# Kernel optimization log

Measured on AMD Instinct MI355X. Metric: run time of the kernel, lower is better.

Reference implementation:

```python
import jax, jax.numpy as jnp
import numpy as np

B, N, D = 4, 2048, 1024
HEADS, DIM_HEAD = 16, 64
INNER = HEADS * DIM_HEAD  # 1024
SCALE = DIM_HEAD ** -0.5


def setup_inputs() -> dict:
    key = jax.random.key(0)
    ks = jax.random.split(key, 8)
    w = 0.02
    return {
        "x":  jax.random.normal(ks[0], (B, N, D), dtype=jnp.float32),
        "Wq": jax.random.normal(ks[1], (D, INNER), dtype=jnp.float32) * w,
        "bq": jax.random.normal(ks[2], (INNER,), dtype=jnp.float32) * w,
        "Wv": jax.random.normal(ks[3], (D, INNER), dtype=jnp.float32) * w,
        "bv": jax.random.normal(ks[4], (INNER,), dtype=jnp.float32) * w,
        "Wo": jax.random.normal(ks[5], (INNER, D), dtype=jnp.float32) * w,
        "bo": jax.random.normal(ks[6], (D,), dtype=jnp.float32) * w,
    }


def reference(x, Wq, bq, Wv, bv, Wo, bo):
    b, n, _ = x.shape
    q = x @ Wq + bq                      # [b, n, inner]
    v = x @ Wv + bv                      # [b, n, inner]
    # split heads -> [b, h, n, d]
    q = q.reshape(b, n, HEADS, DIM_HEAD).transpose(0, 2, 1, 3).astype(jnp.float32)
    v = v.reshape(b, n, HEADS, DIM_HEAD).transpose(0, 2, 1, 3)
    # k = q (self L2 attention)
    AB = jnp.einsum('bhid,bhjd->bhij', q, q)          # [b, h, n, n]
    AA = jnp.sum(q * q, axis=-1, keepdims=True)       # [b, h, n, 1]
    BB = jnp.swapaxes(AA, -1, -2)                     # [b, h, 1, n]
    sim = -(AA - 2.0 * AB + BB) * SCALE               # negative scaled L2 distance
    attn = jax.nn.softmax(sim, axis=-1)
    out = jnp.einsum('bhij,bhjd->bhid', attn, v)      # [b, h, n, d]
    out = out.transpose(0, 2, 1, 3).reshape(b, n, INNER)
    return out @ Wo + bo
```

## Files before the change

### kernel.cpp

```cpp
#include <hip/hip_runtime.h>
#include <hip/hip_bf16.h>

#define SEQ 2048
#define SCALE 0.125f
#define LOG2E 1.4426950408889634f
#define ALPHA 0.6005612049f

typedef __bf16 bf16;
typedef __bf16 bf16x4 __attribute__((ext_vector_type(4)));
typedef __bf16 bf16x8 __attribute__((ext_vector_type(8)));
typedef _Float16 f16;
typedef _Float16 f16x2 __attribute__((ext_vector_type(2)));
typedef _Float16 f16x4 __attribute__((ext_vector_type(4)));
typedef _Float16 f16x8 __attribute__((ext_vector_type(8)));
typedef float f32x4 __attribute__((ext_vector_type(4)));
typedef unsigned int u32;
typedef unsigned int u32x2 __attribute__((ext_vector_type(2)));
typedef unsigned int u32x4 __attribute__((ext_vector_type(4)));

__device__ __forceinline__ f16x2 pk_f16(float a, float b) {
    return __builtin_bit_cast(f16x2, __builtin_amdgcn_cvt_pkrtz(a, b));
}

__device__ __forceinline__ u32 pk_u32(float a, float b) {
    return __builtin_bit_cast(u32, __builtin_amdgcn_cvt_pkrtz(a, b));
}

__device__ __forceinline__ f32x4 mfma_f16_32(f16x8 a, f16x8 b, f32x4 c) {
    return __builtin_amdgcn_mfma_f32_16x16x32_f16(a, b, c, 0, 0, 0);
}

__device__ __forceinline__ void gl_lds16(const void* g, void* l) {
    __builtin_amdgcn_global_load_lds((const __attribute__((address_space(1))) u32*)g,
                                     (__attribute__((address_space(3))) u32*)l, 16, 0, 0);
}


__global__ __launch_bounds__(256) void k_cast_x(const float4* __restrict__ x,
                                                bf16x4* __restrict__ xb) {
    int t = blockIdx.x * 256 + threadIdx.x;
    float4 f = x[t];
    bf16x4 o;
    o[0] = (bf16)f.x; o[1] = (bf16)f.y; o[2] = (bf16)f.z; o[3] = (bf16)f.w;
    xb[t] = o;
}

__global__ __launch_bounds__(256) void k_transpose_cast(const float* __restrict__ src,
                                                        bf16* __restrict__ dst) {
    __shared__ float tile[32][33];
    int bx = blockIdx.x * 32;
    int by = blockIdx.y * 32;
    int tx = threadIdx.x;
    int ty = threadIdx.y;
#pragma unroll
    for (int j = 0; j < 32; j += 8)
        tile[ty + j][tx] = src[(size_t)(by + ty + j) * 1024 + bx + tx];
    __syncthreads();
#pragma unroll
    for (int j = 0; j < 32; j += 8)
        dst[(size_t)(bx + ty + j) * 1024 + by + tx] = (bf16)tile[tx][ty + j];
}


__global__ __launch_bounds__(256) void k_gemm_qv(const bf16* __restrict__ Xb,
                                                 const bf16* __restrict__ Wqvt,
                                                 const float* __restrict__ bq,
                                                 const float* __restrict__ bv,
                                                 bf16* __restrict__ Q,
                                                 f16* __restrict__ Vt,
                                                 float* __restrict__ QN) {
    constexpr int K = 1024;
    __shared__ bf16 As[128 * 32];
    __shared__ bf16 Bs[128 * 32];
    int t = threadIdx.x, w = t >> 6, l = t & 63;
    int blockN = blockIdx.x * 128, blockM = blockIdx.y * 128;
    int wm = w & 1, wn = w >> 1;
    int lr = l & 15, quad = l >> 4, q8 = quad * 8;
    int skcol = (l & 3) * 8;
    bool isQ = blockN < 1024;

    f32x4 acc[4][4] = {};
    const bf16* Ab = Xb + (size_t)blockM * K;
    const bf16* Bb = Wqvt + (size_t)blockN * K;

    for (int k0 = 0; k0 < K; k0 += 32) {
#pragma unroll
        for (int c2 = 0; c2 < 2; ++c2) {
            int c = 2 * w + c2;
            int row = c * 16 + (l >> 2);
            gl_lds16(Ab + (size_t)row * K + k0 + skcol, As + c * 512);
            gl_lds16(Bb + (size_t)row * K + k0 + skcol, Bs + c * 512);
        }
        __syncthreads();
        const bf16* Aw = As + wm * 64 * 32;
        const bf16* Bw = Bs + wn * 64 * 32;
        bf16x8 af[4], bfr[4];
#pragma unroll
        for (int mi = 0; mi < 4; ++mi) af[mi] = *(const bf16x8*)(Aw + (mi * 16 + lr) * 32 + q8);
#pragma unroll
        for (int ni = 0; ni < 4; ++ni) bfr[ni] = *(const bf16x8*)(Bw + (ni * 16 + lr) * 32 + q8);
        if (isQ) {
#pragma unroll
            for (int mi = 0; mi < 4; ++mi)
#pragma unroll
                for (int ni = 0; ni < 4; ++ni)
                    acc[mi][ni] = __builtin_amdgcn_mfma_f32_16x16x32_bf16(af[mi], bfr[ni], acc[mi][ni], 0, 0, 0);
        } else {
#pragma unroll
            for (int mi = 0; mi < 4; ++mi)
#pragma unroll
                for (int ni = 0; ni < 4; ++ni)
                    acc[mi][ni] = __builtin_amdgcn_mfma_f32_16x16x32_bf16(bfr[ni], af[mi], acc[mi][ni], 0, 0, 0);
        }
        __syncthreads();
    }

    int colbase = blockN + wn * 64;
    if (isQ) {
        int h = colbase >> 6;
        float bias[4];
#pragma unroll
        for (int ni = 0; ni < 4; ++ni) bias[ni] = bq[colbase + ni * 16 + lr];
#pragma unroll
        for (int mi = 0; mi < 4; ++mi) {
#pragma unroll
            for (int r = 0; r < 4; ++r) {
                int m = blockM + wm * 64 + mi * 16 + quad * 4 + r;
                int b = m >> 11, s = m & 2047;
                int bh = (b << 4) + h;
                float qsq = 0.f;
#pragma unroll
                for (int ni = 0; ni < 4; ++ni) {
                    float v = (acc[mi][ni][r] + bias[ni]) * ALPHA;
                    bf16 vb = (bf16)v;
                    Q[((size_t)bh * SEQ + s) * 64 + ni * 16 + lr] = vb;
                    float vr = (float)vb;
                    qsq += vr * vr;
                }
                qsq += __shfl_xor(qsq, 1);
                qsq += __shfl_xor(qsq, 2);
                qsq += __shfl_xor(qsq, 4);
                qsq += __shfl_xor(qsq, 8);
                if (lr == 0) QN[(size_t)bh * SEQ + s] = -0.5f * qsq;
            }
        }
    } else {
        int h = (colbase - 1024) >> 6;
        int b = blockM >> 11;
        int bh = (b << 4) + h;
        int s_base = (blockM & 2047) + wm * 64;
        const float* bvh = bv + (colbase - 1024);
#pragma unroll
        for (int ni = 0; ni < 4; ++ni) {
#pragma unroll
            for (int r = 0; r < 4; ++r) {
                int dh = ni * 16 + quad * 4 + r;
                float bias = bvh[dh];
#pragma unroll
                for (int mi = 0; mi < 4; ++mi) {
                    int s = s_base + mi * 16 + lr;
                    Vt[((size_t)bh * 64 + dh) * SEQ + s] = (f16)(acc[mi][ni][r] + bias);
                }
            }
        }
    }
}


__global__ __launch_bounds__(128, 4) void k_attn(const bf16* __restrict__ Q,
                                                 const f16* __restrict__ Vt,
                                                 const float* __restrict__ QN,
                                                 bf16* __restrict__ AO) {
    __shared__ bf16 Ks[64 * 64];
    __shared__ f16 Vs[64 * 64];

    int t = threadIdx.x, w = t >> 6, l = t & 63;
    int bh = blockIdx.y;
    int i0 = blockIdx.x * 64;
    const bf16* Qh = Q + (size_t)bh * SEQ * 64;
    const f16* Vh = Vt + (size_t)bh * 64 * SEQ;
    const float* QNh = QN + (size_t)bh * SEQ;
    int lr = l & 15, quad = l >> 4, q8 = quad * 8, lr7 = lr & 7;

    bf16x8 af[2][2];
#pragma unroll
    for (int mi = 0; mi < 2; ++mi)
#pragma unroll
        for (int kc = 0; kc < 2; ++kc)
            af[mi][kc] = *(const bf16x8*)(Qh + (size_t)(i0 + w * 32 + mi * 16 + lr) * 64 + kc * 32 + q8);

    f32x4 oacc[2][4] = {};
    f32x4 dacc[2] = {};
    const f16x8 ones8 = {(f16)1.f, (f16)1.f, (f16)1.f, (f16)1.f,
                         (f16)1.f, (f16)1.f, (f16)1.f, (f16)1.f};

    int kb[2];
#pragma unroll
    for (int kc = 0; kc < 2; ++kc) kb[kc] = lr * 64 + (((kc * 4 + quad) ^ lr7) * 8);
    int voff[4];
#pragma unroll
    for (int di = 0; di < 4; ++di) voff[di] = (di * 16 + lr) * 64;
    int npo[2];
#pragma unroll
    for (int np = 0; np < 2; ++np) npo[np] = ((np * 4 + quad) ^ lr7) * 8;

    int sr = t >> 3, sc = t & 7;
    int srr[4], sl[4];
#pragma unroll
    for (int i = 0; i < 4; ++i) {
        srr[i] = sr + 16 * i;
        sl[i] = srr[i] * 64 + ((sc ^ (srr[i] & 7)) * 8);
    }

    u32x4 rk[4], rv[4];
#pragma unroll
    for (int i = 0; i < 4; ++i) {
        rk[i] = *(const u32x4*)(Qh + (size_t)srr[i] * 64 + sc * 8);
        rv[i] = *(const u32x4*)(Vh + (size_t)srr[i] * SEQ + sc * 8);
    }

    for (int j0 = 0; j0 < SEQ; j0 += 64) {
        __syncthreads();
#pragma unroll
        for (int i = 0; i < 4; ++i) {
            *(u32x4*)(Ks + sl[i]) = rk[i];
            *(u32x4*)(Vs + sl[i]) = rv[i];
        }
        int jn = j0 + 64;
        if (jn < SEQ) {
#pragma unroll
            for (int i = 0; i < 4; ++i) {
                rk[i] = *(const u32x4*)(Qh + (size_t)(jn + srr[i]) * 64 + sc * 8);
                rv[i] = *(const u32x4*)(Vh + (size_t)srr[i] * SEQ + jn + sc * 8);
            }
        }
        __syncthreads();

#pragma unroll
        for (int np = 0; np < 2; ++np) {
            u32 hA[2][2], hB[2][2];
#pragma unroll
            for (int ni1 = 0; ni1 < 2; ++ni1) {
                int ni = np * 2 + ni1;
                bf16x8 bk0 = *(const bf16x8*)(Ks + ni * 1024 + kb[0]);
                bf16x8 bk1 = *(const bf16x8*)(Ks + ni * 1024 + kb[1]);
                f32x4 bbt = *(const f32x4*)(QNh + j0 + ni * 16 + quad * 4);
                f32x4 sT0 = bbt, sT1 = bbt;
                __builtin_amdgcn_s_setprio(1);
                sT0 = __builtin_amdgcn_mfma_f32_16x16x32_bf16(bk0, af[0][0], sT0, 0, 0, 0);
                sT0 = __builtin_amdgcn_mfma_f32_16x16x32_bf16(bk1, af[0][1], sT0, 0, 0, 0);
                sT1 = __builtin_amdgcn_mfma_f32_16x16x32_bf16(bk0, af[1][0], sT1, 0, 0, 0);
                sT1 = __builtin_amdgcn_mfma_f32_16x16x32_bf16(bk1, af[1][1], sT1, 0, 0, 0);
                __builtin_amdgcn_s_setprio(0);

                float p00 = __builtin_amdgcn_exp2f(sT0[0]);
                float p01 = __builtin_amdgcn_exp2f(sT0[1]);
                float p02 = __builtin_amdgcn_exp2f(sT0[2]);
                float p03 = __builtin_amdgcn_exp2f(sT0[3]);
                float p10 = __builtin_amdgcn_exp2f(sT1[0]);
                float p11 = __builtin_amdgcn_exp2f(sT1[1]);
                float p12 = __builtin_amdgcn_exp2f(sT1[2]);
                float p13 = __builtin_amdgcn_exp2f(sT1[3]);

                hA[ni1][0] = pk_u32(p00, p01);
                hA[ni1][1] = pk_u32(p02, p03);
                hB[ni1][0] = pk_u32(p10, p11);
                hB[ni1][1] = pk_u32(p12, p13);
            }
            f16x8 F8[2];
            {
                u32 a0 = hA[0][0], b0 = hA[1][0], a1 = hA[0][1], b1 = hA[1][1];
                asm("v_permlane32_swap_b32 %0, %1" : "+v"(a0), "+v"(b0));
                asm("v_permlane16_swap_b32 %0, %1" : "+v"(a0), "+v"(b0));
                asm("v_permlane32_swap_b32 %0, %1" : "+v"(a1), "+v"(b1));
                asm("v_permlane16_swap_b32 %0, %1" : "+v"(a1), "+v"(b1));
                u32x4 fu = {a0, a1, b0, b1};
                F8[0] = __builtin_bit_cast(f16x8, fu);
            }
            {
                u32 a0 = hB[0][0], b0 = hB[1][0], a1 = hB[0][1], b1 = hB[1][1];
                asm("v_permlane32_swap_b32 %0, %1" : "+v"(a0), "+v"(b0));
                asm("v_permlane16_swap_b32 %0, %1" : "+v"(a0), "+v"(b0));
                asm("v_permlane32_swap_b32 %0, %1" : "+v"(a1), "+v"(b1));
                asm("v_permlane16_swap_b32 %0, %1" : "+v"(a1), "+v"(b1));
                u32x4 fu = {a0, a1, b0, b1};
                F8[1] = __builtin_bit_cast(f16x8, fu);
            }

            __builtin_amdgcn_s_setprio(1);
            dacc[0] = mfma_f16_32(F8[0], ones8, dacc[0]);
            dacc[1] = mfma_f16_32(F8[1], ones8, dacc[1]);

#pragma unroll
            for (int di = 0; di < 4; ++di) {
                f16x8 vf8 = *(const f16x8*)(Vs + voff[di] + npo[np]);
                oacc[0][di] = mfma_f16_32(F8[0], vf8, oacc[0][di]);
                oacc[1][di] = mfma_f16_32(F8[1], vf8, oacc[1][di]);
            }
            __builtin_amdgcn_s_setprio(0);
        }
    }

    int b = bh >> 4, h = bh & 15;
#pragma unroll
    for (int mi = 0; mi < 2; ++mi) {
#pragma unroll
        for (int r = 0; r < 4; ++r) {
            float inv = 1.f / dacc[mi][r];
            int s = i0 + w * 32 + mi * 16 + quad * 4 + r;
#pragma unroll
            for (int di = 0; di < 4; ++di) {
                AO[((size_t)(b * SEQ + s)) * 1024 + h * 64 + di * 16 + lr] = (bf16)(oacc[mi][di][r] * inv);
            }
        }
    }
}


__global__ __launch_bounds__(256) void k_gemm_out(const bf16* __restrict__ AO,
                                                  const bf16* __restrict__ Wot,
                                                  const float* __restrict__ bo,
                                                  float* __restrict__ out) {
    constexpr int K = 1024;
    __shared__ bf16 As[128 * 32];
    __shared__ bf16 Bs[128 * 32];
    int t = threadIdx.x, w = t >> 6, l = t & 63;
    int blockN = blockIdx.x * 128, blockM = blockIdx.y * 128;
    int wm = w & 1, wn = w >> 1;
    int lr = l & 15, quad = l >> 4, q8 = quad * 8;
    int skcol = (l & 3) * 8;

    f32x4 acc[4][4] = {};
    const bf16* Ab = AO + (size_t)blockM * K;
    const bf16* Bb = Wot + (size_t)blockN * K;

    for (int k0 = 0; k0 < K; k0 += 32) {
#pragma unroll
        for (int c2 = 0; c2 < 2; ++c2) {
            int c = 2 * w + c2;
            int row = c * 16 + (l >> 2);
            gl_lds16(Ab + (size_t)row * K + k0 + skcol, As + c * 512);
            gl_lds16(Bb + (size_t)row * K + k0 + skcol, Bs + c * 512);
        }
        __syncthreads();
        const bf16* Aw = As + wm * 64 * 32;
        const bf16* Bw = Bs + wn * 64 * 32;
        bf16x8 af[4], bfr[4];
#pragma unroll
        for (int mi = 0; mi < 4; ++mi) af[mi] = *(const bf16x8*)(Aw + (mi * 16 + lr) * 32 + q8);
#pragma unroll
        for (int ni = 0; ni < 4; ++ni) bfr[ni] = *(const bf16x8*)(Bw + (ni * 16 + lr) * 32 + q8);
#pragma unroll
        for (int mi = 0; mi < 4; ++mi)
#pragma unroll
            for (int ni = 0; ni < 4; ++ni)
                acc[mi][ni] = __builtin_amdgcn_mfma_f32_16x16x32_bf16(af[mi], bfr[ni], acc[mi][ni], 0, 0, 0);
        __syncthreads();
    }

    int colbase = blockN + wn * 64;
    float bias[4];
#pragma unroll
    for (int ni = 0; ni < 4; ++ni) bias[ni] = bo[colbase + ni * 16 + lr];
#pragma unroll
    for (int mi = 0; mi < 4; ++mi) {
#pragma unroll
        for (int r = 0; r < 4; ++r) {
            int m = blockM + wm * 64 + mi * 16 + quad * 4 + r;
#pragma unroll
            for (int ni = 0; ni < 4; ++ni) {
                out[(size_t)m * 1024 + colbase + ni * 16 + lr] = acc[mi][ni][r] + bias[ni];
            }
        }
    }
}


extern "C" void kernel_launch(void* const* d_in, const int* in_sizes, int n_in,
                              void* d_out, int out_size, void* d_ws, size_t ws_size,
                              hipStream_t stream) {
    const float* x  = (const float*)d_in[0];
    const float* Wq = (const float*)d_in[1];
    const float* bq = (const float*)d_in[2];
    const float* Wv = (const float*)d_in[3];
    const float* bv = (const float*)d_in[4];
    const float* Wo = (const float*)d_in[5];
    const float* bo = (const float*)d_in[6];
    float* out = (float*)d_out;

    char* ws = (char*)d_ws;
    bf16* Xb   = (bf16*)ws;
    bf16* Wqvt = (bf16*)(ws + (size_t)(16 << 20));
    bf16* Wot  = (bf16*)(ws + (size_t)(20 << 20));
    bf16* Qb   = (bf16*)(ws + (size_t)(22 << 20));
    f16*  Vtb  = (f16*)(ws + (size_t)(38 << 20));
    float* QN  = (float*)(ws + (size_t)(54 << 20));
    bf16* AO   = Xb;

    k_cast_x<<<8192, 256, 0, stream>>>((const float4*)x, (bf16x4*)Xb);
    dim3 tb(32, 8);
    k_transpose_cast<<<dim3(32, 32), tb, 0, stream>>>(Wq, Wqvt);
    k_transpose_cast<<<dim3(32, 32), tb, 0, stream>>>(Wv, Wqvt + 1024 * 1024);
    k_transpose_cast<<<dim3(32, 32), tb, 0, stream>>>(Wo, Wot);
    k_gemm_qv<<<dim3(16, 64), 256, 0, stream>>>(Xb, Wqvt, bq, bv, Qb, Vtb, QN);
    k_attn<<<dim3(32, 64), 128, 0, stream>>>(Qb, Vtb, QN, AO);
    k_gemm_out<<<dim3(8, 64), 256, 0, stream>>>(AO, Wot, bo, out);
}
```

Before: 313.0 us.

## Double attention query tile per wave and stage key norms in LDS

After: 279.4 us. 10.7% less time.

```diff
diff --git a/kernel.cpp b/kernel.cpp
--- a/kernel.cpp
+++ b/kernel.cpp
@@ -17,10 +17,6 @@
 typedef unsigned int u32;
 typedef unsigned int u32x2 __attribute__((ext_vector_type(2)));
 typedef unsigned int u32x4 __attribute__((ext_vector_type(4)));
-
-__device__ __forceinline__ f16x2 pk_f16(float a, float b) {
-    return __builtin_bit_cast(f16x2, __builtin_amdgcn_cvt_pkrtz(a, b));
-}
 
 __device__ __forceinline__ u32 pk_u32(float a, float b) {
     return __builtin_bit_cast(u32, __builtin_amdgcn_cvt_pkrtz(a, b));
@@ -167,30 +163,39 @@
 }
 
 
-__global__ __launch_bounds__(128, 4) void k_attn(const bf16* __restrict__ Q,
+__global__ __launch_bounds__(128, 2) void k_attn(const bf16* __restrict__ Q,
                                                  const f16* __restrict__ Vt,
                                                  const float* __restrict__ QN,
                                                  bf16* __restrict__ AO) {
     __shared__ bf16 Ks[64 * 64];
     __shared__ f16 Vs[64 * 64];
+    __shared__ float BBl[2048];
 
     int t = threadIdx.x, w = t >> 6, l = t & 63;
     int bh = blockIdx.y;
-    int i0 = blockIdx.x * 64;
+    int i0 = blockIdx.x * 128;
     const bf16* Qh = Q + (size_t)bh * SEQ * 64;
     const f16* Vh = Vt + (size_t)bh * 64 * SEQ;
-    const float* QNh = QN + (size_t)bh * SEQ;
     int lr = l & 15, quad = l >> 4, q8 = quad * 8, lr7 = lr & 7;
 
-    bf16x8 af[2][2];
-#pragma unroll
-    for (int mi = 0; mi < 2; ++mi)
+    {
+        const float4* QN4 = (const float4*)(QN + (size_t)bh * SEQ);
+        float4* BB4 = (float4*)BBl;
+        BB4[t] = QN4[t];
+        BB4[t + 128] = QN4[t + 128];
+        BB4[t + 256] = QN4[t + 256];
+        BB4[t + 384] = QN4[t + 384];
+    }
+
+    bf16x8 af[4][2];
+#pragma unroll
+    for (int mi = 0; mi < 4; ++mi)
 #pragma unroll
         for (int kc = 0; kc < 2; ++kc)
-            af[mi][kc] = *(const bf16x8*)(Qh + (size_t)(i0 + w * 32 + mi * 16 + lr) * 64 + kc * 32 + q8);
-
-    f32x4 oacc[2][4] = {};
-    f32x4 dacc[2] = {};
+            af[mi][kc] = *(const bf16x8*)(Qh + (size_t)(i0 + w * 64 + mi * 16 + lr) * 64 + kc * 32 + q8);
+
+    f32x4 oacc[4][4] = {};
+    f32x4 dacc[4] = {};
     const f16x8 ones8 = {(f16)1.f, (f16)1.f, (f16)1.f, (f16)1.f,
                          (f16)1.f, (f16)1.f, (f16)1.f, (f16)1.f};
 
@@ -238,79 +243,62 @@
 
 #pragma unroll
         for (int np = 0; np < 2; ++np) {
-            u32 hA[2][2], hB[2][2];
+            u32 h[4][2][2];
 #pragma unroll
             for (int ni1 = 0; ni1 < 2; ++ni1) {
                 int ni = np * 2 + ni1;
                 bf16x8 bk0 = *(const bf16x8*)(Ks + ni * 1024 + kb[0]);
                 bf16x8 bk1 = *(const bf16x8*)(Ks + ni * 1024 + kb[1]);
-                f32x4 bbt = *(const f32x4*)(QNh + j0 + ni * 16 + quad * 4);
-                f32x4 sT0 = bbt, sT1 = bbt;
-                __builtin_amdgcn_s_setprio(1);
-                sT0 = __builtin_amdgcn_mfma_f32_16x16x32_bf16(bk0, af[0][0], sT0, 0, 0, 0);
-                sT0 = __builtin_amdgcn_mfma_f32_16x16x32_bf16(bk1, af[0][1], sT0, 0, 0, 0);
-                sT1 = __builtin_amdgcn_mfma_f32_16x16x32_bf16(bk0, af[1][0], sT1, 0, 0, 0);
-                sT1 = __builtin_amdgcn_mfma_f32_16x16x32_bf16(bk1, af[1][1], sT1, 0, 0, 0);
-                __builtin_amdgcn_s_setprio(0);
-
-                float p00 = __builtin_amdgcn_exp2f(sT0[0]);
-                float p01 = __builtin_amdgcn_exp2f(sT0[1]);
-                float p02 = __builtin_amdgcn_exp2f(sT0[2]);
-                float p03 = __builtin_amdgcn_exp2f(sT0[3]);
-                float p10 = __builtin_amdgcn_exp2f(sT1[0]);
-                float p11 = __builtin_amdgcn_exp2f(sT1[1]);
-                float p12 = __builtin_amdgcn_exp2f(sT1[2]);
-                float p13 = __builtin_amdgcn_exp2f(sT1[3]);
-
-                hA[ni1][0] = pk_u32(p00, p01);
-                hA[ni1][1] = pk_u32(p02, p03);
-                hB[ni1][0] = pk_u32(p10, p11);
-                hB[ni1][1] = pk_u32(p12, p13);
-            }
-            f16x8 F8[2];
-            {
-                u32 a0 = hA[0][0], b0 = hA[1][0], a1 = hA[0][1], b1 = hA[1][1];
+                f32x4 bbt = *(const f32x4*)(BBl + j0 + ni * 16 + quad * 4);
+#pragma unroll
+                for (int mi = 0; mi < 4; ++mi) {
+                    f32x4 sT = __builtin_amdgcn_mfma_f32_16x16x32_bf16(bk0, af[mi][0], bbt, 0, 0, 0);
+                    sT = __builtin_amdgcn_mfma_f32_16x16x32_bf16(bk1, af[mi][1], sT, 0, 0, 0);
+                    float p0 = __builtin_amdgcn_exp2f(sT[0]);
+                    float p1 = __builtin_amdgcn_exp2f(sT[1]);
+                    float p2 = __builtin_amdgcn_exp2f(sT[2]);
+                    float p3 = __builtin_amdgcn_exp2f(sT[3]);
+                    h[mi][ni1][0] = pk_u32(p0, p1);
+                    h[mi][ni1][1] = pk_u32(p2, p3);
+                }
+            }
+            f16x8 F8[4];
+#pragma unroll
+            for (int mi = 0; mi < 4; ++mi) {
+                u32 a0 = h[mi][0][0], b0 = h[mi][1][0], a1 = h[mi][0][1], b1 = h[mi][1][1];
                 asm("v_permlane32_swap_b32 %0, %1" : "+v"(a0), "+v"(b0));
                 asm("v_permlane16_swap_b32 %0, %1" : "+v"(a0), "+v"(b0));
                 asm("v_permlane32_swap_b32 %0, %1" : "+v"(a1), "+v"(b1));
                 asm("v_permlane16_swap_b32 %0, %1" : "+v"(a1), "+v"(b1));
                 u32x4 fu = {a0, a1, b0, b1};
-                F8[0] = __builtin_bit_cast(f16x8, fu);
-            }
-            {
-                u32 a0 = hB[0][0], b0 = hB[1][0], a1 = hB[0][1], b1 = hB[1][1];
-                asm("v_permlane32_swap_b32 %0, %1" : "+v"(a0), "+v"(b0));
-                asm("v_permlane16_swap_b32 %0, %1" : "+v"(a0), "+v"(b0));
-                asm("v_permlane32_swap_b32 %0, %1" : "+v"(a1), "+v"(b1));
-                asm("v_permlane16_swap_b32 %0, %1" : "+v"(a1), "+v"(b1));
-                u32x4 fu = {a0, a1, b0, b1};
-                F8[1] = __builtin_bit_cast(f16x8, fu);
+                F8[mi] = __builtin_bit_cast(f16x8, fu);
             }
 
             __builtin_amdgcn_s_setprio(1);
-            dacc[0] = mfma_f16_32(F8[0], ones8, dacc[0]);
-            dacc[1] = mfma_f16_32(F8[1], ones8, dacc[1]);
-
+#pragma unroll
+            for (int mi = 0; mi < 4; ++mi)
+                dacc[mi] = mfma_f16_32(F8[mi], ones8, dacc[mi]);
 #pragma unroll
             for (int di = 0; di < 4; ++di) {
                 f16x8 vf8 = *(const f16x8*)(Vs + voff[di] + npo[np]);
-                oacc[0][di] = mfma_f16_32(F8[0], vf8, oacc[0][di]);
-                oacc[1][di] = mfma_f16_32(F8[1], vf8, oacc[1][di]);
+#pragma unroll
+                for (int mi = 0; mi < 4; ++mi)
+                    oacc[mi][di] = mfma_f16_32(F8[mi], vf8, oacc[mi][di]);
             }
             __builtin_amdgcn_s_setprio(0);
         }
     }
 
-    int b = bh >> 4, h = bh & 15;
-#pragma unroll
-    for (int mi = 0; mi < 2; ++mi) {
+    int b = bh >> 4, hh = bh & 15;
+#pragma unroll
+    for (int mi = 0; mi < 4; ++mi) {
 #pragma unroll
         for (int r = 0; r < 4; ++r) {
             float inv = 1.f / dacc[mi][r];
-            int s = i0 + w * 32 + mi * 16 + quad * 4 + r;
+            int s = i0 + w * 64 + mi * 16 + quad * 4 + r;
 #pragma unroll
             for (int di = 0; di < 4; ++di) {
-                AO[((size_t)(b * SEQ + s)) * 1024 + h * 64 + di * 16 + lr] = (bf16)(oacc[mi][di][r] * inv);
+                AO[((size_t)(b * SEQ + s)) * 1024 + hh * 64 + di * 16 + lr] = (bf16)(oacc[mi][di][r] * inv);
             }
         }
     }
@@ -403,6 +391,6 @@
     k_transpose_cast<<<dim3(32, 32), tb, 0, stream>>>(Wv, Wqvt + 1024 * 1024);
     k_transpose_cast<<<dim3(32, 32), tb, 0, stream>>>(Wo, Wot);
     k_gemm_qv<<<dim3(16, 64), 256, 0, stream>>>(Xb, Wqvt, bq, bv, Qb, Vtb, QN);
-    k_attn<<<dim3(32, 64), 128, 0, stream>>>(Qb, Vtb, QN, AO);
+    k_attn<<<dim3(16, 64), 128, 0, stream>>>(Qb, Vtb, QN, AO);
     k_gemm_out<<<dim3(8, 64), 256, 0, stream>>>(AO, Wot, bo, out);
 }
```
